# Kernel tuning notes

Hardware: AMD Instinct MI355X
Metric: run time of the kernel (lower is better)

Reference implementation:

```python
import jax, jax.numpy as jnp
import numpy as np

B = 1048576
INDIM = 10
DIM = 32
LAYERS = 4
MODES = DIM // 2 + 1  # 17 rfft modes


def setup_inputs() -> dict:
    key = jax.random.key(0)
    ks = jax.random.split(key, 10)
    scale = 1.0 / (DIM * DIM)
    inp = {
        "x": jax.random.normal(ks[0], (B, INDIM), dtype=jnp.float32),
        # stem: Linear(indim, dim), stored as [in, out]
        "stem_W": jax.random.normal(ks[1], (INDIM, DIM), dtype=jnp.float32) / np.sqrt(INDIM),
        "stem_b": jnp.zeros((DIM,), dtype=jnp.float32),
        # per-layer complex spectral weights, stored as real/imag parts [L, modes, modes]
        "fno_wr": scale * jax.random.uniform(ks[2], (LAYERS, MODES, MODES), dtype=jnp.float32),
        "fno_wi": scale * jax.random.uniform(ks[3], (LAYERS, MODES, MODES), dtype=jnp.float32),
        # per-layer proj: Linear(dim, dim), stored as [L, in, out]
        "proj_W": jax.random.normal(ks[4], (LAYERS, DIM, DIM), dtype=jnp.float32) / np.sqrt(DIM),
        "proj_b": jnp.zeros((LAYERS, DIM), dtype=jnp.float32),
        # head: Linear(dim, indim)
        "head_W": jax.random.normal(ks[5], (DIM, INDIM), dtype=jnp.float32) / np.sqrt(DIM),
        "head_b": jnp.zeros((INDIM,), dtype=jnp.float32),
    }
    return inp


def reference(x, stem_W, stem_b, fno_wr, fno_wi, proj_W, proj_b, head_W, head_b):
    # stem
    h = x @ stem_W + stem_b  # [B, DIM]
    for i in range(LAYERS):
        w = fno_wr[i] + 1j * fno_wi[i]  # [MODES, MODES] complex64
        hf = jnp.fft.rfft(h, axis=-1)  # [B, MODES] complex
        # complex linear mix of modes (bias=False since condition_num=0)
        x1 = jnp.fft.irfft(jnp.einsum('bi,io->bo', hf, w), axis=-1)  # [B, DIM]
        x2 = h @ proj_W[i] + proj_b[i]  # [B, DIM]
        h = jax.nn.silu(x1 + x2)
    return h @ head_W + head_b  # [B, INDIM]
```

## Files before the change

### kernel.cpp

```cpp
#include <hip/hip_runtime.h>
#include <math.h>

#define INDIM 10
#define DIM 32
#define LAYERS 4
#define MODES 17

#define LOG2E 1.4426950408889634f
#define LN2   0.6931471805599453f

#define WS_FRAG_OFF 0
#define WS_BIAS_OFF 11264

typedef _Float16 f16;
typedef _Float16 f16x8 __attribute__((ext_vector_type(8)));
typedef float f32x16 __attribute__((ext_vector_type(16)));
typedef unsigned u32x2 __attribute__((ext_vector_type(2)));

union BU { f16x8 v; unsigned u[4]; };
union CU { f32x16 v; float4 q[4]; };

__global__ void fno_prep(const float* __restrict__ wr,
                         const float* __restrict__ wi,
                         const float* __restrict__ projW,
                         const float* __restrict__ stemW,
                         const float* __restrict__ headW,
                         const float* __restrict__ stemB,
                         const float* __restrict__ projB,
                         const float* __restrict__ headB,
                         f16* __restrict__ frag,
                         float* __restrict__ bias2) {
    const int l  = blockIdx.x;
    const int tx = threadIdx.x;
    const int j  = tx & 31;
    const int n  = tx >> 5;

    __shared__ float ct[32], st[32];
    if (tx < 32) {
        float ang = (2.0f * 3.14159265358979323846f / 32.0f) * (float)tx;
        ct[tx] = cosf(ang);
        st[tx] = sinf(ang);
    }
    __syncthreads();

    const float* lwr = wr + l * MODES * MODES;
    const float* lwi = wi + l * MODES * MODES;

    float acc = 0.0f;
    for (int o = 0; o < MODES; ++o) {
        float re = 0.0f, im = 0.0f;
        for (int m = 0; m < MODES; ++m) {
            int t = (m * n) & 31;
            float c = ct[t], s = st[t];
            float a = lwr[m * MODES + o];
            float b = lwi[m * MODES + o];
            re += c * a + s * b;
            im += c * b - s * a;
        }
        int t2 = (o * j) & 31;
        float f = (o == 0 || o == 16) ? 1.0f : 2.0f;
        acc += f * (re * ct[t2] - im * st[t2]);
    }
    acc = acc * (1.0f / 32.0f) + projW[(l * DIM + n) * DIM + j];

    const float wscale = (l == 0) ? LOG2E : 1.0f;
    const int kc = n >> 4;
    const int G  = (n >> 3) & 1;
    const int e  = n & 7;
    const int ln = G * 32 + j;
    frag[((l * 2 + kc) * 64 + ln) * 8 + e] = (f16)(wscale * acc);

    if (l == 0) {
        if (tx < 64) {
            const int lnn = tx;
            const int c2  = lnn & 31;
            const int G2  = lnn >> 5;
#pragma unroll
            for (int ee = 0; ee < 8; ++ee) {
                int k = 8 * G2 + ee;
                frag[(8 * 64 + lnn) * 8 + ee] =
                    (f16)(k < INDIM ? stemW[k * DIM + c2] : 0.0f);
            }
#pragma unroll
            for (int kcc = 0; kcc < 2; ++kcc)
#pragma unroll
                for (int ee = 0; ee < 8; ++ee) {
                    int k = 16 * kcc + 8 * G2 + ee;
                    frag[((9 + kcc) * 64 + lnn) * 8 + ee] =
                        (f16)(c2 < INDIM ? LN2 * headW[k * INDIM + c2] : 0.0f);
                }
        }
        if (tx < 32) {
#pragma unroll
            for (int f = 0; f < 6; ++f) {
                float v;
                if (f == 0)      v = stemB[tx];
                else if (f <= 4) v = LOG2E * projB[(f - 1) * DIM + tx];
                else             v = (tx < INDIM) ? headB[tx] : 0.0f;
                bias2[f * 32 + tx] = v;
            }
        }
    }
}

__device__ __forceinline__ float exp2_fast(float x) {
#if __has_builtin(__builtin_amdgcn_exp2f)
    return __builtin_amdgcn_exp2f(x);
#else
    return exp2f(x);
#endif
}

__device__ __forceinline__ unsigned pk2(float a, float b) {
    auto h2 = __builtin_amdgcn_cvt_pkrtz(a, b);
    return __builtin_bit_cast(unsigned, h2);
}

__device__ __forceinline__ void pswap(unsigned& a, unsigned& b) {
#if __has_builtin(__builtin_amdgcn_permlane32_swap)
    u32x2 r = __builtin_amdgcn_permlane32_swap(a, b, false, false);
    a = r[0];
    b = r[1];
#else
    asm("v_permlane32_swap_b32 %0, %1" : "+v"(a), "+v"(b));
    __builtin_amdgcn_sched_barrier(0);
#endif
}

template <bool SILU>
__device__ __forceinline__ void pack_exchange_dual(const f32x16& DA, const f32x16& DB,
                                                   BU& a0, BU& a1, BU& b0, BU& b1) {
    float sA[16], sB[16];
    if (SILU) {
        float uA[16], uB[16];
#pragma unroll
        for (int r = 0; r < 16; ++r) uA[r] = exp2_fast(-DA[r]);
#pragma unroll
        for (int r = 0; r < 16; ++r) uB[r] = exp2_fast(-DB[r]);
#pragma unroll
        for (int r = 0; r < 16; ++r) uA[r] = 1.0f + uA[r];
#pragma unroll
        for (int r = 0; r < 16; ++r) uB[r] = 1.0f + uB[r];
#pragma unroll
        for (int r = 0; r < 16; ++r) uA[r] = __builtin_amdgcn_rcpf(uA[r]);
#pragma unroll
        for (int r = 0; r < 16; ++r) uB[r] = __builtin_amdgcn_rcpf(uB[r]);
#pragma unroll
        for (int r = 0; r < 16; ++r) sA[r] = DA[r] * uA[r];
#pragma unroll
        for (int r = 0; r < 16; ++r) sB[r] = DB[r] * uB[r];
    } else {
#pragma unroll
        for (int r = 0; r < 16; ++r) { sA[r] = DA[r]; sB[r] = DB[r]; }
    }

    unsigned qa0 = pk2(sA[0],  sA[1]);
    unsigned qa1 = pk2(sA[2],  sA[3]);
    unsigned qa2 = pk2(sA[4],  sA[5]);
    unsigned qa3 = pk2(sA[6],  sA[7]);
    unsigned qa4 = pk2(sA[8],  sA[9]);
    unsigned qa5 = pk2(sA[10], sA[11]);
    unsigned qa6 = pk2(sA[12], sA[13]);
    unsigned qa7 = pk2(sA[14], sA[15]);
    unsigned qb0 = pk2(sB[0],  sB[1]);
    unsigned qb1 = pk2(sB[2],  sB[3]);
    unsigned qb2 = pk2(sB[4],  sB[5]);
    unsigned qb3 = pk2(sB[6],  sB[7]);
    unsigned qb4 = pk2(sB[8],  sB[9]);
    unsigned qb5 = pk2(sB[10], sB[11]);
    unsigned qb6 = pk2(sB[12], sB[13]);
    unsigned qb7 = pk2(sB[14], sB[15]);
    pswap(qa0, qa2); pswap(qa1, qa3); pswap(qa4, qa6); pswap(qa5, qa7);
    pswap(qb0, qb2); pswap(qb1, qb3); pswap(qb4, qb6); pswap(qb5, qb7);
    a0.u[0] = qa0; a0.u[1] = qa1; a0.u[2] = qa2; a0.u[3] = qa3;
    a1.u[0] = qa4; a1.u[1] = qa5; a1.u[2] = qa6; a1.u[3] = qa7;
    b0.u[0] = qb0; b0.u[1] = qb1; b0.u[2] = qb2; b0.u[3] = qb3;
    b1.u[0] = qb4; b1.u[1] = qb5; b1.u[2] = qb6; b1.u[3] = qb7;
}

__device__ __forceinline__ f32x16 ld_bias(const float* sbias, int stage, int G) {
    CU c;
#pragma unroll
    for (int rq = 0; rq < 4; ++rq)
        c.q[rq] = *(const float4*)&sbias[stage * 32 + rq * 8 + G * 4];
    return c.v;
}

template <bool GUARD>
__device__ __forceinline__ BU load_x(const float* __restrict__ x, long rb,
                                     int c, int G, int nrows) {
    BU b;
    b.u[0] = 0; b.u[1] = 0; b.u[2] = 0; b.u[3] = 0;
    const long r = rb + c;
    if (!GUARD || r < nrows) {
        const float* xp = x + r * INDIM;
        if (G == 0) {
            float2 p0 = *(const float2*)(xp + 0);
            float2 p1 = *(const float2*)(xp + 2);
            float2 p2 = *(const float2*)(xp + 4);
            float2 p3 = *(const float2*)(xp + 6);
            b.u[0] = pk2(p0.x, p0.y);
            b.u[1] = pk2(p1.x, p1.y);
            b.u[2] = pk2(p2.x, p2.y);
            b.u[3] = pk2(p3.x, p3.y);
        } else {
            float2 p4 = *(const float2*)(xp + 8);
            b.u[0] = pk2(p4.x, p4.y);
        }
    }
    return b;
}

template <bool GUARD>
__device__ __forceinline__ void store_o(float* __restrict__ out, long rb,
                                        int c, int G, int nrows, const f32x16& Dh) {
    const long r = rb + c;
    if (!GUARD || r < nrows) {
        float* op = out + r * INDIM;
        if (G == 0) {
            *(float2*)(op + 0) = make_float2(Dh[0], Dh[1]);
            *(float2*)(op + 2) = make_float2(Dh[2], Dh[3]);
            *(float2*)(op + 8) = make_float2(Dh[4], Dh[5]);
        } else {
            *(float2*)(op + 4) = make_float2(Dh[0], Dh[1]);
            *(float2*)(op + 6) = make_float2(Dh[2], Dh[3]);
        }
    }
}

template <bool GUARD>
__global__ __launch_bounds__(256, 3) void fno_main(
    const float* __restrict__ x,
    const f16*  __restrict__ fragbuf,
    const float* __restrict__ bias2,
    float* __restrict__ out,
    int nrows) {

    __shared__ __align__(16) float sbias[6 * 32];
    if (threadIdx.x < 6 * 32) sbias[threadIdx.x] = bias2[threadIdx.x];
    __syncthreads();

    const int tid = threadIdx.x;
    const int w   = tid >> 6;
    const int ln  = tid & 63;
    const int c   = ln & 31;
    const int G   = ln >> 5;

    const f16x8* fb = (const f16x8*)fragbuf;
    f16x8 wa[2 * LAYERS];
#pragma unroll
    for (int f = 0; f < 2 * LAYERS; ++f) wa[f] = fb[f * 64 + ln];
    const f16x8 as  = fb[8 * 64 + ln];
    const f16x8 ah0 = fb[9 * 64 + ln];
    const f16x8 ah1 = fb[10 * 64 + ln];

    const long rbA = (long)blockIdx.x * 256 + (long)w * 64;
    const long rbB = rbA + 32;

    BU bxA = load_x<GUARD>(x, rbA, c, G, nrows);
    BU bxB = load_x<GUARD>(x, rbB, c, G, nrows);
    f32x16 cb = ld_bias(sbias, 0, G);
    f32x16 DA = __builtin_amdgcn_mfma_f32_32x32x16_f16(as, bxA.v, cb, 0, 0, 0);
    f32x16 DB = __builtin_amdgcn_mfma_f32_32x32x16_f16(as, bxB.v, cb, 0, 0, 0);
    cb = ld_bias(sbias, 1, G);

    BU a0, a1, b0, b1;
    pack_exchange_dual<false>(DA, DB, a0, a1, b0, b1);

#pragma unroll
    for (int l = 0; l < LAYERS; ++l) {
        f32x16 tA = __builtin_amdgcn_mfma_f32_32x32x16_f16(wa[2 * l], a0.v, cb, 0, 0, 0);
        f32x16 tB = __builtin_amdgcn_mfma_f32_32x32x16_f16(wa[2 * l], b0.v, cb, 0, 0, 0);
        tA = __builtin_amdgcn_mfma_f32_32x32x16_f16(wa[2 * l + 1], a1.v, tA, 0, 0, 0);
        tB = __builtin_amdgcn_mfma_f32_32x32x16_f16(wa[2 * l + 1], b1.v, tB, 0, 0, 0);
        cb = ld_bias(sbias, (l < LAYERS - 1) ? (2 + l) : 5, G);
        pack_exchange_dual<true>(tA, tB, a0, a1, b0, b1);
    }

    f32x16 HA = __builtin_amdgcn_mfma_f32_32x32x16_f16(ah0, a0.v, cb, 0, 0, 0);
    f32x16 HB = __builtin_amdgcn_mfma_f32_32x32x16_f16(ah0, b0.v, cb, 0, 0, 0);
    HA = __builtin_amdgcn_mfma_f32_32x32x16_f16(ah1, a1.v, HA, 0, 0, 0);
    HB = __builtin_amdgcn_mfma_f32_32x32x16_f16(ah1, b1.v, HB, 0, 0, 0);

    store_o<GUARD>(out, rbA, c, G, nrows, HA);
    store_o<GUARD>(out, rbB, c, G, nrows, HB);
}

extern "C" void kernel_launch(void* const* d_in, const int* in_sizes, int n_in,
                              void* d_out, int out_size, void* d_ws, size_t ws_size,
                              hipStream_t stream) {
    const float* x      = (const float*)d_in[0];
    const float* stemW  = (const float*)d_in[1];
    const float* stemB  = (const float*)d_in[2];
    const float* fno_wr = (const float*)d_in[3];
    const float* fno_wi = (const float*)d_in[4];
    const float* projW  = (const float*)d_in[5];
    const float* projB  = (const float*)d_in[6];
    const float* headW  = (const float*)d_in[7];
    const float* headB  = (const float*)d_in[8];
    float* out = (float*)d_out;

    f16*   frag  = (f16*)((char*)d_ws + WS_FRAG_OFF);
    float* bias2 = (float*)((char*)d_ws + WS_BIAS_OFF);

    const int nrows = in_sizes[0] / INDIM;

    fno_prep<<<LAYERS, 1024, 0, stream>>>(fno_wr, fno_wi, projW, stemW, headW,
                                          stemB, projB, headB, frag, bias2);

    const int rows_per_block = 256;
    const int nblk = (nrows + rows_per_block - 1) / rows_per_block;
    if (nrows % rows_per_block == 0)
        fno_main<false><<<nblk, 256, 0, stream>>>(x, frag, bias2, out, nrows);
    else
        fno_main<true><<<nblk, 256, 0, stream>>>(x, frag, bias2, out, nrows);
}
```

Measured before the change: 57.98 us.

## Stage MFMA weight fragments in LDS and raise occupancy to four blocks

Weight fragments that each wave previously held in registers (eleven f16x8 vectors per lane) are now copied once per block into shared memory and read from LDS just before each MFMA. This frees VGPRs, and the launch bounds are raised from 3 to 4 blocks per CU to use the lower register pressure for higher occupancy. The cost is extra LDS reads on the critical path of each layer and an initial cooperative copy per block. The bias load is also vectorized to float4.

New measurement: 60.77 us. +4.8%, slower.

```diff
diff --git a/kernel.cpp b/kernel.cpp
--- a/kernel.cpp
+++ b/kernel.cpp
@@ -186,6 +186,10 @@
     return c.v;
 }
 
+__device__ __forceinline__ f16x8 ld_frag(const f16* sfrag, int f, int ln) {
+    return *(const f16x8*)&sfrag[(f * 64 + ln) * 8];
+}
+
 template <bool GUARD>
 __device__ __forceinline__ BU load_x(const float* __restrict__ x, long rb,
                                      int c, int G, int nrows) {
@@ -229,15 +233,27 @@
 }
 
 template <bool GUARD>
-__global__ __launch_bounds__(256, 3) void fno_main(
+__global__ __launch_bounds__(256, 4) void fno_main(
     const float* __restrict__ x,
     const f16*  __restrict__ fragbuf,
     const float* __restrict__ bias2,
     float* __restrict__ out,
     int nrows) {
 
+    __shared__ __align__(16) f16 sfrag[11 * 64 * 8];
     __shared__ __align__(16) float sbias[6 * 32];
-    if (threadIdx.x < 6 * 32) sbias[threadIdx.x] = bias2[threadIdx.x];
+
+    {
+        const int tid = threadIdx.x;
+        uint4* dv = (uint4*)sfrag;
+        const uint4* sv = (const uint4*)fragbuf;
+#pragma unroll
+        for (int i = 0; i < 3; ++i) {
+            int idx = tid + i * 256;
+            if (idx < 704) dv[idx] = sv[idx];
+        }
+        if (tid < 48) ((float4*)sbias)[tid] = ((const float4*)bias2)[tid];
+    }
     __syncthreads();
 
     const int tid = threadIdx.x;
@@ -246,20 +262,13 @@
     const int c   = ln & 31;
     const int G   = ln >> 5;
 
-    const f16x8* fb = (const f16x8*)fragbuf;
-    f16x8 wa[2 * LAYERS];
-#pragma unroll
-    for (int f = 0; f < 2 * LAYERS; ++f) wa[f] = fb[f * 64 + ln];
-    const f16x8 as  = fb[8 * 64 + ln];
-    const f16x8 ah0 = fb[9 * 64 + ln];
-    const f16x8 ah1 = fb[10 * 64 + ln];
-
     const long rbA = (long)blockIdx.x * 256 + (long)w * 64;
     const long rbB = rbA + 32;
 
     BU bxA = load_x<GUARD>(x, rbA, c, G, nrows);
     BU bxB = load_x<GUARD>(x, rbB, c, G, nrows);
     f32x16 cb = ld_bias(sbias, 0, G);
+    f16x8 as = ld_frag(sfrag, 8, ln);
     f32x16 DA = __builtin_amdgcn_mfma_f32_32x32x16_f16(as, bxA.v, cb, 0, 0, 0);
     f32x16 DB = __builtin_amdgcn_mfma_f32_32x32x16_f16(as, bxB.v, cb, 0, 0, 0);
     cb = ld_bias(sbias, 1, G);
@@ -269,14 +278,18 @@
 
 #pragma unroll
     for (int l = 0; l < LAYERS; ++l) {
-        f32x16 tA = __builtin_amdgcn_mfma_f32_32x32x16_f16(wa[2 * l], a0.v, cb, 0, 0, 0);
-        f32x16 tB = __builtin_amdgcn_mfma_f32_32x32x16_f16(wa[2 * l], b0.v, cb, 0, 0, 0);
-        tA = __builtin_amdgcn_mfma_f32_32x32x16_f16(wa[2 * l + 1], a1.v, tA, 0, 0, 0);
-        tB = __builtin_amdgcn_mfma_f32_32x32x16_f16(wa[2 * l + 1], b1.v, tB, 0, 0, 0);
+        f16x8 w0 = ld_frag(sfrag, 2 * l, ln);
+        f16x8 w1 = ld_frag(sfrag, 2 * l + 1, ln);
+        f32x16 tA = __builtin_amdgcn_mfma_f32_32x32x16_f16(w0, a0.v, cb, 0, 0, 0);
+        f32x16 tB = __builtin_amdgcn_mfma_f32_32x32x16_f16(w0, b0.v, cb, 0, 0, 0);
+        tA = __builtin_amdgcn_mfma_f32_32x32x16_f16(w1, a1.v, tA, 0, 0, 0);
+        tB = __builtin_amdgcn_mfma_f32_32x32x16_f16(w1, b1.v, tB, 0, 0, 0);
         cb = ld_bias(sbias, (l < LAYERS - 1) ? (2 + l) : 5, G);
         pack_exchange_dual<true>(tA, tB, a0, a1, b0, b1);
     }
 
+    f16x8 ah0 = ld_frag(sfrag, 9, ln);
+    f16x8 ah1 = ld_frag(sfrag, 10, ln);
     f32x16 HA = __builtin_amdgcn_mfma_f32_32x32x16_f16(ah0, a0.v, cb, 0, 0, 0);
     f32x16 HB = __builtin_amdgcn_mfma_f32_32x32x16_f16(ah0, b0.v, cb, 0, 0, 0);
     HA = __builtin_amdgcn_mfma_f32_32x32x16_f16(ah1, a1.v, HA, 0, 0, 0);
```
